# Kernel optimization log

Measured on AMD Instinct MI355X. Metric: run time of the kernel, lower is better.

Reference implementation:

```python
import jax, jax.numpy as jnp
import numpy as np

D = 1024
H = 16
FF = 4 * D


def layer_norm(x, g, b, eps=1e-5):
    mu = jnp.mean(x, axis=-1, keepdims=True)
    var = jnp.var(x, axis=-1, keepdims=True)
    return (x - mu) * jax.lax.rsqrt(var + eps) * g + b


def setup_inputs() -> dict:
    key = jax.random.key(0)
    ks = jax.random.split(key, 8)
    s = lambda fan_in: 1.0 / np.sqrt(fan_in)
    return {
        "x": jax.random.normal(ks[0], (2, 2048, D), dtype=jnp.float32),
        "ln1_g": jnp.ones((D,), jnp.float32),
        "ln1_b": jnp.zeros((D,), jnp.float32),
        "w_qkv": jax.random.uniform(ks[1], (D, 3 * D), jnp.float32, -s(D), s(D)),
        "b_qkv": jnp.zeros((3 * D,), jnp.float32),
        "w_out": jax.random.uniform(ks[2], (D, D), jnp.float32, -s(D), s(D)),
        "b_out": jnp.zeros((D,), jnp.float32),
        "ln2_g": jnp.ones((D,), jnp.float32),
        "ln2_b": jnp.zeros((D,), jnp.float32),
        "w_fc1": jax.random.uniform(ks[3], (D, FF), jnp.float32, -s(D), s(D)),
        "b_fc1": jnp.zeros((FF,), jnp.float32),
        "w_fc2": jax.random.uniform(ks[4], (FF, D), jnp.float32, -s(FF), s(FF)),
        "b_fc2": jnp.zeros((D,), jnp.float32),
    }


def reference(x, ln1_g, ln1_b, w_qkv, b_qkv, w_out, b_out,
              ln2_g, ln2_b, w_fc1, b_fc1, w_fc2, b_fc2):
    b, n, c = x.shape
    hd = c // H
    scale = hd ** -0.5

    # --- pre-norm MHA ---
    h = layer_norm(x, ln1_g, ln1_b)
    qkv = h @ w_qkv + b_qkv                      # [b,n,3c]
    qkv = qkv.reshape(b, n, 3, H, hd)
    q = jnp.transpose(qkv[:, :, 0], (0, 2, 1, 3))  # [b,H,n,hd]
    k = jnp.transpose(qkv[:, :, 1], (0, 2, 1, 3))
    v = jnp.transpose(qkv[:, :, 2], (0, 2, 1, 3))
    attn = jnp.einsum('bhqd,bhkd->bhqk', q, k) * scale
    attn = jax.nn.softmax(attn, axis=-1)
    o = jnp.einsum('bhqk,bhkd->bhqd', attn, v)   # [b,H,n,hd]
    o = jnp.transpose(o, (0, 2, 1, 3)).reshape(b, n, c)
    x = x + (o @ w_out + b_out)

    # --- pre-norm FFN ---
    h = layer_norm(x, ln2_g, ln2_b)
    h = jax.nn.gelu(h @ w_fc1 + b_fc1, approximate=False)
    x = x + (h @ w_fc2 + b_fc2)
    return x
```

## Files before the change

kernel.cpp:

```cpp
#include <hip/hip_runtime.h>
#include <stdint.h>
#include <math.h>

#define D_MODEL 1024
#define NHEAD   16
#define HDIM    64
#define FFDIM   4096
#define SEQ     2048
#define BATCH   2
#define NTOK    (BATCH*SEQ)
#define QKVN    (3*D_MODEL)

typedef __bf16 bf16;
typedef __attribute__((ext_vector_type(8))) __bf16 bf16x8;
typedef __attribute__((ext_vector_type(4))) __bf16 bf16x4;
typedef __attribute__((ext_vector_type(4))) float f32x4;

__device__ __forceinline__ void gld_lds16(const void* g, void* l) {
    __builtin_amdgcn_global_load_lds((__attribute__((address_space(1))) void*)g,
                                     (__attribute__((address_space(3))) void*)l,
                                     16, 0, 0);
}

__device__ __forceinline__ float fast_exp2(float x) {
#if __has_builtin(__builtin_amdgcn_exp2f)
    return __builtin_amdgcn_exp2f(x);
#else
    return __expf(x * 0.69314718056f);
#endif
}

__device__ __forceinline__ float fast_rcp(float x) {
#if __has_builtin(__builtin_amdgcn_rcpf)
    return __builtin_amdgcn_rcpf(x);
#else
    return 1.0f / x;
#endif
}

__device__ __forceinline__ float gelu_fast(float x) {
    float xx = x * x;
    float y  = x * fmaf(0.035677408137f, xx, 0.7978845608f);
    float z  = fminf(-2.8853900817779268f * y, 126.0f);
    float e  = fast_exp2(z);
    return x * fast_rcp(1.0f + e);
}

#define BARRIER() do {                                         \
    __builtin_amdgcn_s_barrier();                              \
    asm volatile("" ::: "memory");                             \
} while (0)
#define LGKM0() asm volatile("s_waitcnt lgkmcnt(0)" ::: "memory")
#define VMW(N)  asm volatile("s_waitcnt vmcnt(" #N ")" ::: "memory")

#define PHASE_BAR() do {                                       \
    asm volatile("s_waitcnt vmcnt(0)" ::: "memory");           \
    __builtin_amdgcn_s_barrier();                              \
    asm volatile("" ::: "memory");                             \
} while (0)

__global__ __launch_bounds__(256)
void k_transpose_all(const float* __restrict__ w_qkv, const float* __restrict__ w_out,
                     const float* __restrict__ w_fc1, const float* __restrict__ w_fc2,
                     bf16* __restrict__ t_qkv, bf16* __restrict__ t_out,
                     bf16* __restrict__ t_fc1, bf16* __restrict__ t_fc2) {
    __shared__ float tile[32][33];
    int bid = blockIdx.x;
    const float* W; bf16* Wt; int K, N, ti;
    if (bid < 3072)       { W = w_qkv; Wt = t_qkv; K = 1024; N = 3072; ti = bid; }
    else if (bid < 4096)  { W = w_out; Wt = t_out; K = 1024; N = 1024; ti = bid - 3072; }
    else if (bid < 8192)  { W = w_fc1; Wt = t_fc1; K = 1024; N = 4096; ti = bid - 4096; }
    else                  { W = w_fc2; Wt = t_fc2; K = 4096; N = 1024; ti = bid - 8192; }
    int tn = N >> 5;
    int n0 = (ti % tn) * 32, k0 = (ti / tn) * 32;
    int tx = threadIdx.x, ty = threadIdx.y;
#pragma unroll
    for (int i = 0; i < 4; i++)
        tile[ty + i * 8][tx] = W[(size_t)(k0 + ty + i * 8) * N + n0 + tx];
    __syncthreads();
#pragma unroll
    for (int i = 0; i < 4; i++)
        Wt[(size_t)(n0 + ty + i * 8) * K + k0 + tx] = (bf16)tile[tx][ty + i * 8];
}

__global__ __launch_bounds__(256)
void k_vtrans(const bf16* __restrict__ qkv, bf16* __restrict__ vT) {
    __shared__ bf16 t[32][33];
    int tok0 = blockIdx.x * 32, f0 = blockIdx.y * 32;
    int tx = threadIdx.x, ty = threadIdx.y;
#pragma unroll
    for (int i = 0; i < 4; i++)
        t[ty + i * 8][tx] = qkv[(size_t)(tok0 + ty + i * 8) * QKVN + 2 * D_MODEL + f0 + tx];
    __syncthreads();
    int s = tx;
    int pp = (s < 16) ? ((s >> 2) * 8 + (s & 3))
                      : (((s - 16) >> 2) * 8 + ((s - 16) & 3) + 4);
#pragma unroll
    for (int i = 0; i < 4; i++)
        vT[(size_t)(f0 + ty + i * 8) * NTOK + tok0 + pp] = t[tx][ty + i * 8];
}

__global__ __launch_bounds__(256)
void k_layernorm(const float* __restrict__ x, const float* __restrict__ g,
                 const float* __restrict__ b, bf16* __restrict__ out) {
    int row = blockIdx.x;
    int tid = threadIdx.x;
    float4 v = ((const float4*)(x + (size_t)row * D_MODEL))[tid];
    float s  = v.x + v.y + v.z + v.w;
    float ss = v.x * v.x + v.y * v.y + v.z * v.z + v.w * v.w;
#pragma unroll
    for (int off = 32; off > 0; off >>= 1) {
        s  += __shfl_down(s, off, 64);
        ss += __shfl_down(ss, off, 64);
    }
    __shared__ float red[2][4];
    __shared__ float mv[2];
    int wave = tid >> 6, lane = tid & 63;
    if (lane == 0) { red[0][wave] = s; red[1][wave] = ss; }
    __syncthreads();
    if (tid == 0) {
        float S  = red[0][0] + red[0][1] + red[0][2] + red[0][3];
        float SS = red[1][0] + red[1][1] + red[1][2] + red[1][3];
        float mu = S * (1.0f / D_MODEL);
        float var = SS * (1.0f / D_MODEL) - mu * mu;
        mv[0] = mu;
        mv[1] = rsqrtf(var + 1e-5f);
    }
    __syncthreads();
    float mu = mv[0], rs = mv[1];
    float4 gv = ((const float4*)g)[tid];
    float4 bv = ((const float4*)b)[tid];
    bf16x4 ov = { (bf16)((v.x - mu) * rs * gv.x + bv.x),
                  (bf16)((v.y - mu) * rs * gv.y + bv.y),
                  (bf16)((v.z - mu) * rs * gv.z + bv.z),
                  (bf16)((v.w - mu) * rs * gv.w + bv.w) };
    *(bf16x4*)(out + (size_t)row * D_MODEL + tid * 4) = ov;
}

template <int DO_GELU>
__global__ __launch_bounds__(512, 2)
void k_gemm256(const bf16* __restrict__ A, const bf16* __restrict__ Bt,
               const float* __restrict__ bias, bf16* __restrict__ outb,
               int M, int N, int K) {
    __shared__ bf16 LA[2][2][8192];
    __shared__ bf16 LB[2][2][8192];

    int tid = threadIdx.x;
    int wid = tid >> 6, lane = tid & 63;
    int quad = lane >> 4, l16 = lane & 15;
    int wm = (wid >> 2) * 128;
    int wn = (wid & 3) * 64;

    int nwg = gridDim.x * gridDim.y;
    int bid = blockIdx.y * gridDim.x + blockIdx.x;
    int sid = (bid & 7) * (nwg >> 3) + (bid >> 3);
    int bx = sid % gridDim.x, by = sid / gridDim.x;
    int m0 = by * 256, n0 = bx * 256;

    int l = lane;
    int rsw = l >> 2;
    int csw = 8 * ((l & 3) ^ ((l >> 3) & 3));
    const bf16* pA = A  + (size_t)(m0 + 32 * wid + rsw) * K + csw;
    const bf16* pB = Bt + (size_t)(n0 + 32 * wid + rsw) * K + csw;
    int sbase = wid * 1024;

    int xq = 8 * (quad ^ ((l16 >> 1) & 3));

    f32x4 acc[8][4];
#pragma unroll
    for (int i = 0; i < 8; i++)
#pragma unroll
        for (int j = 0; j < 4; j++) acc[i][j] = (f32x4){0.f, 0.f, 0.f, 0.f};

#define STAGE_A(buf, kh, t) do {                                               \
    gld_lds16(pA + (size_t)(t) * 64 + (kh) * 32,              &LA[buf][kh][sbase]);       \
    gld_lds16(pA + (size_t)16 * K + (size_t)(t) * 64 + (kh) * 32, &LA[buf][kh][sbase + 512]); \
} while (0)
#define STAGE_B(buf, kh, t) do {                                               \
    gld_lds16(pB + (size_t)(t) * 64 + (kh) * 32,              &LB[buf][kh][sbase]);       \
    gld_lds16(pB + (size_t)16 * K + (size_t)(t) * 64 + (kh) * 32, &LB[buf][kh][sbase + 512]); \
} while (0)

    bf16x8 af[4], bfr[4];
#define RD_B(buf, kh)  do {                                                    \
    _Pragma("unroll")                                                          \
    for (int fc = 0; fc < 4; fc++)                                             \
        bfr[fc] = *(const bf16x8*)&LB[buf][kh][(wn + fc * 16 + l16) * 32 + xq];\
} while (0)
#define RD_A(buf, kh, rh) do {                                                 \
    _Pragma("unroll")                                                          \
    for (int fr = 0; fr < 4; fr++)                                             \
        af[fr] = *(const bf16x8*)&LA[buf][kh][(wm + (rh) * 64 + fr * 16 + l16) * 32 + xq]; \
} while (0)
#define MFMA16(rh) do {                                                        \
    __builtin_amdgcn_s_setprio(1);                                             \
    _Pragma("unroll")                                                          \
    for (int fr = 0; fr < 4; fr++)                                             \
        _Pragma("unroll")                                                      \
        for (int fc = 0; fc < 4; fc++)                                         \
            acc[(rh) * 4 + fr][fc] =                                           \
                __builtin_amdgcn_mfma_f32_16x16x32_bf16(af[fr], bfr[fc],       \
                                                        acc[(rh) * 4 + fr][fc], 0, 0, 0); \
    __builtin_amdgcn_s_setprio(0);                                             \
} while (0)

    int nt = K / 64;
    int buf = 0;
    STAGE_A(0, 0, 0); STAGE_B(0, 0, 0);
    STAGE_A(0, 1, 0); STAGE_B(0, 1, 0);
    STAGE_A(1, 0, 1); STAGE_B(1, 0, 1);
    VMW(8); BARRIER();

    for (int t = 0; t < nt - 1; t++) {
        int ts = (t + 2 < nt) ? (t + 2) : (nt - 1);
        RD_B(buf, 0); RD_A(buf, 0, 0);
        STAGE_A(buf ^ 1, 1, t + 1);
        BARRIER(); LGKM0();
        MFMA16(0);
        BARRIER();
        RD_A(buf, 0, 1);
        STAGE_B(buf ^ 1, 1, t + 1);
        BARRIER(); LGKM0();
        MFMA16(1);
        VMW(8); BARRIER();
        RD_B(buf, 1); RD_A(buf, 1, 0);
        STAGE_A(buf, 0, ts);
        BARRIER(); LGKM0();
        MFMA16(0);
        BARRIER();
        RD_A(buf, 1, 1);
        STAGE_B(buf, 0, ts);
        BARRIER(); LGKM0();
        MFMA16(1);
        VMW(8); BARRIER();
        buf ^= 1;
    }
    RD_B(buf, 0); RD_A(buf, 0, 0);
    BARRIER(); LGKM0();
    MFMA16(0);
    BARRIER();
    RD_A(buf, 0, 1);
    BARRIER(); LGKM0();
    MFMA16(1);
    VMW(4); BARRIER();
    RD_B(buf, 1); RD_A(buf, 1, 0);
    BARRIER(); LGKM0();
    MFMA16(0);
    BARRIER();
    RD_A(buf, 1, 1);
    LGKM0();
    MFMA16(1);
    VMW(0);

#undef STAGE_A
#undef STAGE_B
#undef RD_A
#undef RD_B
#undef MFMA16

#pragma unroll
    for (int fi = 0; fi < 8; fi++) {
        int row = m0 + wm + fi * 16 + quad * 4;
#pragma unroll
        for (int fc = 0; fc < 4; fc++) {
            int col = n0 + wn + fc * 16 + l16;
            float bb = bias[col];
#pragma unroll
            for (int r = 0; r < 4; r++) {
                float v = acc[fi][fc][r] + bb;
                if (DO_GELU) v = gelu_fast(v);
                outb[(size_t)(row + r) * N + col] = (bf16)v;
            }
        }
    }
}

__global__ __launch_bounds__(256, 3)
void k_gemm128x64(const bf16* __restrict__ A, const bf16* __restrict__ Bt,
                  const float* __restrict__ bias, const float* res,
                  float* outf, int M, int N, int K) {
    __shared__ bf16 LA[2][2][4096];
    __shared__ bf16 LB[2][2][2048];

    int tid = threadIdx.x;
    int wid = tid >> 6, lane = tid & 63;
    int quad = lane >> 4, l16 = lane & 15;
    int wm = (wid >> 1) * 64;
    int wn = (wid & 1) * 32;

    int nwg = gridDim.x * gridDim.y;
    int bid = blockIdx.y * gridDim.x + blockIdx.x;
    int sid = (bid & 7) * (nwg >> 3) + (bid >> 3);
    int bx = sid % gridDim.x, by = sid / gridDim.x;
    int m0 = by * 128, n0 = bx * 64;

    int l = lane;
    int rsw = l >> 2;
    int csw = 8 * ((l & 3) ^ ((l >> 3) & 3));
    const bf16* pA = A  + (size_t)(m0 + 32 * wid + rsw) * K + csw;
    const bf16* pB = Bt + (size_t)(n0 + 16 * wid + rsw) * K + csw;
    int sbaseA = wid * 1024;
    int sbaseB = wid * 512;

    int xq = 8 * (quad ^ ((l16 >> 1) & 3));

    f32x4 acc[4][2];
#pragma unroll
    for (int i = 0; i < 4; i++)
#pragma unroll
        for (int j = 0; j < 2; j++) acc[i][j] = (f32x4){0.f, 0.f, 0.f, 0.f};

#define STAGE_AB(buf, kh, t) do {                                              \
    gld_lds16(pA + (size_t)(t) * 64 + (kh) * 32,                  &LA[buf][kh][sbaseA]);       \
    gld_lds16(pA + (size_t)16 * K + (size_t)(t) * 64 + (kh) * 32, &LA[buf][kh][sbaseA + 512]); \
    gld_lds16(pB + (size_t)(t) * 64 + (kh) * 32,                  &LB[buf][kh][sbaseB]);       \
} while (0)

    bf16x8 af[4], bfr[2];
#define RD(buf, kh)  do {                                                      \
    _Pragma("unroll")                                                          \
    for (int fc = 0; fc < 2; fc++)                                             \
        bfr[fc] = *(const bf16x8*)&LB[buf][kh][(wn + fc * 16 + l16) * 32 + xq];\
    _Pragma("unroll")                                                          \
    for (int fr = 0; fr < 4; fr++)                                             \
        af[fr] = *(const bf16x8*)&LA[buf][kh][(wm + fr * 16 + l16) * 32 + xq]; \
} while (0)
#define MFMA8() do {                                                           \
    __builtin_amdgcn_s_setprio(1);                                             \
    _Pragma("unroll")                                                          \
    for (int fr = 0; fr < 4; fr++)                                             \
        _Pragma("unroll")                                                      \
        for (int fc = 0; fc < 2; fc++)                                         \
            acc[fr][fc] =                                                      \
                __builtin_amdgcn_mfma_f32_16x16x32_bf16(af[fr], bfr[fc],       \
                                                        acc[fr][fc], 0, 0, 0); \
    __builtin_amdgcn_s_setprio(0);                                             \
} while (0)

    int nt = K / 64;
    int buf = 0;
    STAGE_AB(0, 0, 0);
    STAGE_AB(0, 1, 0);
    STAGE_AB(1, 0, 1);
    VMW(6); BARRIER();

    for (int t = 0; t < nt - 1; t++) {
        int ts = (t + 2 < nt) ? (t + 2) : (nt - 1);
        RD(buf, 0);
        STAGE_AB(buf ^ 1, 1, t + 1);
        BARRIER(); LGKM0();
        MFMA8();
        VMW(6); BARRIER();
        RD(buf, 1);
        STAGE_AB(buf, 0, ts);
        BARRIER(); LGKM0();
        MFMA8();
        VMW(6); BARRIER();
        buf ^= 1;
    }
    RD(buf, 0);
    BARRIER(); LGKM0();
    MFMA8();
    VMW(3); BARRIER();
    RD(buf, 1);
    LGKM0();
    MFMA8();
    VMW(0);

#undef STAGE_AB
#undef RD
#undef MFMA8

#pragma unroll
    for (int fr = 0; fr < 4; fr++) {
        int row = m0 + wm + fr * 16 + quad * 4;
#pragma unroll
        for (int fc = 0; fc < 2; fc++) {
            int col = n0 + wn + fc * 16 + l16;
            float bb = bias[col];
#pragma unroll
            for (int r = 0; r < 4; r++) {
                size_t idx = (size_t)(row + r) * N + col;
                outf[idx] = res[idx] + acc[fr][fc][r] + bb;
            }
        }
    }
}

__global__ __launch_bounds__(256)
void k_attention2(const bf16* __restrict__ qkv, const bf16* __restrict__ vT,
                  bf16* __restrict__ o) {
    __shared__ bf16 Ks[2][2][64][32];
    __shared__ bf16 Vs[2][2][64][32];

    int tid = threadIdx.x, wave = tid >> 6, lane = tid & 63;
    int quad = lane >> 4, l16 = lane & 15;
    int bh = blockIdx.y;
    int b = bh >> 4, h = bh & 15;
    int q0 = blockIdx.x * 64 + wave * 16;

    const bf16* Qb  = qkv + (size_t)b * SEQ * QKVN + h * HDIM;
    const bf16* Kb  = Qb + D_MODEL;
    const bf16* vTb = vT + (size_t)h * HDIM * NTOK + b * SEQ;

    const float QSCALE = 0.125f * 1.44269504089f;
    bf16x8 qf[2];
#pragma unroll
    for (int c = 0; c < 2; c++) {
        bf16x8 qraw = *(const bf16x8*)(Qb + (size_t)(q0 + l16) * QKVN + c * 32 + quad * 8);
#pragma unroll
        for (int i = 0; i < 8; i++) qf[c][i] = (bf16)((float)qraw[i] * QSCALE);
    }

    const bf16* gK0 = Kb + (size_t)(wave * 16 + (lane >> 2)) * QKVN + (lane & 3) * 8;
    const bf16* gK1 = gK0 + 32;
    const bf16* gV0 = vTb + (size_t)(wave * 16 + (lane >> 2)) * NTOK + (lane & 3) * 8;
    const bf16* gV1 = gV0 + 32;

    f32x4 oacc[4];
#pragma unroll
    for (int i = 0; i < 4; i++) oacc[i] = (f32x4){0.f, 0.f, 0.f, 0.f};
    float lsum = 0.f;

    gld_lds16(gK0, &Ks[0][0][wave * 16][0]);
    gld_lds16(gK1, &Ks[0][1][wave * 16][0]);
    gld_lds16(gV0, &Vs[0][0][wave * 16][0]);
    gld_lds16(gV1, &Vs[0][1][wave * 16][0]);
    PHASE_BAR();

    int buf = 0;
    for (int kv0 = 0; kv0 < SEQ; kv0 += 64) {
        if (kv0 + 64 < SEQ) {
            size_t koff = (size_t)(kv0 + 64) * QKVN;
            gld_lds16(gK0 + koff, &Ks[buf ^ 1][0][wave * 16][0]);
            gld_lds16(gK1 + koff, &Ks[buf ^ 1][1][wave * 16][0]);
            gld_lds16(gV0 + kv0 + 64, &Vs[buf ^ 1][0][wave * 16][0]);
            gld_lds16(gV1 + kv0 + 64, &Vs[buf ^ 1][1][wave * 16][0]);
        }

        f32x4 s[4];
#pragma unroll
        for (int t = 0; t < 4; t++) {
            bf16x8 af0 = *(const bf16x8*)(&Ks[buf][0][t * 16 + l16][quad * 8]);
            bf16x8 af1 = *(const bf16x8*)(&Ks[buf][1][t * 16 + l16][quad * 8]);
            f32x4 z = (f32x4){0.f, 0.f, 0.f, 0.f};
            z = __builtin_amdgcn_mfma_f32_16x16x32_bf16(af0, qf[0], z, 0, 0, 0);
            z = __builtin_amdgcn_mfma_f32_16x16x32_bf16(af1, qf[1], z, 0, 0, 0);
            s[t] = z;
        }

        bf16x4 p[4];
#pragma unroll
        for (int t = 0; t < 4; t++)
#pragma unroll
            for (int r = 0; r < 4; r++) {
                float pf = fast_exp2(s[t][r]);
                lsum += pf;
                p[t][r] = (bf16)pf;
            }

#pragma unroll
        for (int tp = 0; tp < 2; tp++) {
            bf16x8 pa = __builtin_shufflevector(p[2 * tp], p[2 * tp + 1], 0, 1, 2, 3, 4, 5, 6, 7);
#pragma unroll
            for (int nt = 0; nt < 4; nt++) {
                bf16x8 vb = *(const bf16x8*)(&Vs[buf][tp][nt * 16 + l16][quad * 8]);
                oacc[nt] = __builtin_amdgcn_mfma_f32_16x16x32_bf16(pa, vb, oacc[nt], 0, 0, 0);
            }
        }

        PHASE_BAR();
        buf ^= 1;
    }

    lsum += __shfl_xor(lsum, 16, 64);
    lsum += __shfl_xor(lsum, 32, 64);
    float invl[4];
#pragma unroll
    for (int r = 0; r < 4; r++)
        invl[r] = 1.0f / __shfl(lsum, quad * 4 + r, 16);

#pragma unroll
    for (int nt = 0; nt < 4; nt++)
#pragma unroll
        for (int r = 0; r < 4; r++)
            o[(size_t)(b * SEQ + q0 + quad * 4 + r) * D_MODEL + h * HDIM + nt * 16 + l16] =
                (bf16)(oacc[nt][r] * invl[r]);
}

extern "C" void kernel_launch(void* const* d_in, const int* in_sizes, int n_in,
                              void* d_out, int out_size, void* d_ws, size_t ws_size,
                              hipStream_t stream) {
    const float* x     = (const float*)d_in[0];
    const float* ln1_g = (const float*)d_in[1];
    const float* ln1_b = (const float*)d_in[2];
    const float* w_qkv = (const float*)d_in[3];
    const float* b_qkv = (const float*)d_in[4];
    const float* w_out = (const float*)d_in[5];
    const float* b_out = (const float*)d_in[6];
    const float* ln2_g = (const float*)d_in[7];
    const float* ln2_b = (const float*)d_in[8];
    const float* w_fc1 = (const float*)d_in[9];
    const float* b_fc1 = (const float*)d_in[10];
    const float* w_fc2 = (const float*)d_in[11];
    const float* b_fc2 = (const float*)d_in[12];
    float* out = (float*)d_out;

    uintptr_t ws = (uintptr_t)d_ws;
    bf16* wt_qkv = (bf16*)(ws + 0);
    bf16* wt_out = (bf16*)(ws + 6291456);
    bf16* wt_fc1 = (bf16*)(ws + 8388608);
    bf16* wt_fc2 = (bf16*)(ws + 16777216);
    bf16* hbuf   = (bf16*)(ws + 25165824);
    bf16* vT     = hbuf;
    bf16* qkv    = (bf16*)(ws + 33554432);
    bf16* attn_o = (bf16*)(ws + 58720256);
    bf16* hgelu  = (bf16*)(ws + 33554432);

    k_transpose_all<<<12288, dim3(32, 8), 0, stream>>>(w_qkv, w_out, w_fc1, w_fc2,
                                                       wt_qkv, wt_out, wt_fc1, wt_fc2);

    k_layernorm<<<NTOK, 256, 0, stream>>>(x, ln1_g, ln1_b, hbuf);

    k_gemm256<0><<<dim3(QKVN / 256, NTOK / 256), 512, 0, stream>>>(
        hbuf, wt_qkv, b_qkv, qkv, NTOK, QKVN, D_MODEL);

    k_vtrans<<<dim3(NTOK / 32, D_MODEL / 32), dim3(32, 8), 0, stream>>>(qkv, vT);

    k_attention2<<<dim3(SEQ / 64, BATCH * NHEAD), 256, 0, stream>>>(qkv, vT, attn_o);

    k_gemm128x64<<<dim3(D_MODEL / 64, NTOK / 128), 256, 0, stream>>>(
        attn_o, wt_out, b_out, x, out, NTOK, D_MODEL, D_MODEL);

    k_layernorm<<<NTOK, 256, 0, stream>>>(out, ln2_g, ln2_b, hbuf);

    k_gemm256<1><<<dim3(FFDIM / 256, NTOK / 256), 512, 0, stream>>>(
        hbuf, wt_fc1, b_fc1, hgelu, NTOK, FFDIM, D_MODEL);

    k_gemm128x64<<<dim3(D_MODEL / 64, NTOK / 128), 256, 0, stream>>>(
        hgelu, wt_fc2, b_fc2, out, out, NTOK, D_MODEL, FFDIM);
}
```

Measured before the change: 344.8 us.

## Triple-buffer K tiles and split barriers in attention pipeline

The attention kernel now keeps three K tile buffers and two V buffers. K is staged two iterations ahead and V one ahead, and a partial vmcnt wait sits between the QK and PV phases in place of a full drain at the end of each iteration. The aim is to hide global-to-LDS load latency behind the MFMA work and stop every iteration from waiting on all outstanding loads. It also adds s_setprio around the MFMA sections. The cost is more LDS use and two barriers per iteration, and the counter-based waits rely on exact ordering of issued loads.

```diff
diff --git a/kernel.cpp b/kernel.cpp
--- a/kernel.cpp
+++ b/kernel.cpp
@@ -52,12 +52,6 @@
 } while (0)
 #define LGKM0() asm volatile("s_waitcnt lgkmcnt(0)" ::: "memory")
 #define VMW(N)  asm volatile("s_waitcnt vmcnt(" #N ")" ::: "memory")
-
-#define PHASE_BAR() do {                                       \
-    asm volatile("s_waitcnt vmcnt(0)" ::: "memory");           \
-    __builtin_amdgcn_s_barrier();                              \
-    asm volatile("" ::: "memory");                             \
-} while (0)
 
 __global__ __launch_bounds__(256)
 void k_transpose_all(const float* __restrict__ w_qkv, const float* __restrict__ w_out,
@@ -390,7 +384,7 @@
 __global__ __launch_bounds__(256)
 void k_attention2(const bf16* __restrict__ qkv, const bf16* __restrict__ vT,
                   bf16* __restrict__ o) {
-    __shared__ bf16 Ks[2][2][64][32];
+    __shared__ bf16 Ks[3][2][64][32];
     __shared__ bf16 Vs[2][2][64][32];
 
     int tid = threadIdx.x, wave = tid >> 6, lane = tid & 63;
@@ -417,61 +411,79 @@
     const bf16* gV0 = vTb + (size_t)(wave * 16 + (lane >> 2)) * NTOK + (lane & 3) * 8;
     const bf16* gV1 = gV0 + 32;
 
+#define STAGE_K(b3, t) do {                                                    \
+    size_t koff_ = (size_t)(t) * 64 * QKVN;                                    \
+    gld_lds16(gK0 + koff_, &Ks[b3][0][wave * 16][0]);                          \
+    gld_lds16(gK1 + koff_, &Ks[b3][1][wave * 16][0]);                          \
+} while (0)
+#define STAGE_V(b2, t) do {                                                    \
+    gld_lds16(gV0 + (t) * 64, &Vs[b2][0][wave * 16][0]);                       \
+    gld_lds16(gV1 + (t) * 64, &Vs[b2][1][wave * 16][0]);                       \
+} while (0)
+
     f32x4 oacc[4];
 #pragma unroll
     for (int i = 0; i < 4; i++) oacc[i] = (f32x4){0.f, 0.f, 0.f, 0.f};
     float lsum = 0.f;
 
-    gld_lds16(gK0, &Ks[0][0][wave * 16][0]);
-    gld_lds16(gK1, &Ks[0][1][wave * 16][0]);
-    gld_lds16(gV0, &Vs[0][0][wave * 16][0]);
-    gld_lds16(gV1, &Vs[0][1][wave * 16][0]);
-    PHASE_BAR();
-
-    int buf = 0;
-    for (int kv0 = 0; kv0 < SEQ; kv0 += 64) {
-        if (kv0 + 64 < SEQ) {
-            size_t koff = (size_t)(kv0 + 64) * QKVN;
-            gld_lds16(gK0 + koff, &Ks[buf ^ 1][0][wave * 16][0]);
-            gld_lds16(gK1 + koff, &Ks[buf ^ 1][1][wave * 16][0]);
-            gld_lds16(gV0 + kv0 + 64, &Vs[buf ^ 1][0][wave * 16][0]);
-            gld_lds16(gV1 + kv0 + 64, &Vs[buf ^ 1][1][wave * 16][0]);
-        }
+    const int NT = SEQ / 64;
+    STAGE_K(0, 0);
+    STAGE_K(1, 1);
+    STAGE_V(0, 0);
+    VMW(4); BARRIER();
+
+    int b3 = 0, b2 = 0;
+    for (int t = 0; t < NT; t++) {
+        if (t + 2 < NT) STAGE_K((t + 2) % 3, t + 2);
+        if (t + 1 < NT) STAGE_V((t + 1) & 1, t + 1);
 
         f32x4 s[4];
-#pragma unroll
-        for (int t = 0; t < 4; t++) {
-            bf16x8 af0 = *(const bf16x8*)(&Ks[buf][0][t * 16 + l16][quad * 8]);
-            bf16x8 af1 = *(const bf16x8*)(&Ks[buf][1][t * 16 + l16][quad * 8]);
+        __builtin_amdgcn_s_setprio(1);
+#pragma unroll
+        for (int tt = 0; tt < 4; tt++) {
+            bf16x8 af0 = *(const bf16x8*)(&Ks[b3][0][tt * 16 + l16][quad * 8]);
+            bf16x8 af1 = *(const bf16x8*)(&Ks[b3][1][tt * 16 + l16][quad * 8]);
             f32x4 z = (f32x4){0.f, 0.f, 0.f, 0.f};
             z = __builtin_amdgcn_mfma_f32_16x16x32_bf16(af0, qf[0], z, 0, 0, 0);
             z = __builtin_amdgcn_mfma_f32_16x16x32_bf16(af1, qf[1], z, 0, 0, 0);
-            s[t] = z;
+            s[tt] = z;
         }
+        __builtin_amdgcn_s_setprio(0);
+
+        if (t + 2 < NT)      { VMW(4); }
+        else if (t + 1 < NT) { VMW(2); }
+        else                 { VMW(0); }
+        BARRIER();
 
         bf16x4 p[4];
 #pragma unroll
-        for (int t = 0; t < 4; t++)
+        for (int tt = 0; tt < 4; tt++)
 #pragma unroll
             for (int r = 0; r < 4; r++) {
-                float pf = fast_exp2(s[t][r]);
+                float pf = fast_exp2(s[tt][r]);
                 lsum += pf;
-                p[t][r] = (bf16)pf;
+                p[tt][r] = (bf16)pf;
             }
 
+        __builtin_amdgcn_s_setprio(1);
 #pragma unroll
         for (int tp = 0; tp < 2; tp++) {
             bf16x8 pa = __builtin_shufflevector(p[2 * tp], p[2 * tp + 1], 0, 1, 2, 3, 4, 5, 6, 7);
 #pragma unroll
             for (int nt = 0; nt < 4; nt++) {
-                bf16x8 vb = *(const bf16x8*)(&Vs[buf][tp][nt * 16 + l16][quad * 8]);
+                bf16x8 vb = *(const bf16x8*)(&Vs[b2][tp][nt * 16 + l16][quad * 8]);
                 oacc[nt] = __builtin_amdgcn_mfma_f32_16x16x32_bf16(pa, vb, oacc[nt], 0, 0, 0);
             }
         }
-
-        PHASE_BAR();
-        buf ^= 1;
-    }
+        __builtin_amdgcn_s_setprio(0);
+
+        BARRIER();
+        b3 = (b3 + 1) % 3;
+        b2 ^= 1;
+    }
+
+#undef STAGE_K
+#undef STAGE_V
 
     lsum += __shfl_xor(lsum, 16, 64);
     lsum += __shfl_xor(lsum, 32, 64);
```

After: 345.9 us. Within noise of the previous version (+0.3%).
